# Kernel optimization log

Hardware: AMD Instinct MI355X
Metric: run time of the kernel (lower is better)

The kernel has to match this reference:

```python
import jax, jax.numpy as jnp
import numpy as np

K = 1024       # num mixture components
D = 6          # state_dim (pos + vel)
B = 16384      # number of query points


def setup_inputs() -> dict:
    key = jax.random.key(0)
    k1, k2, k3, k4 = jax.random.split(key, 4)
    x = jax.random.normal(k1, (B, D), dtype=jnp.float32)
    means = jax.random.normal(k2, (K, D), dtype=jnp.float32)
    # SPD covariances: F @ F^T / D + 0.1 * I
    F = jax.random.normal(k3, (K, D, D), dtype=jnp.float32)
    covs = jnp.einsum('kij,klj->kil', F, F) / D + 0.1 * jnp.eye(D, dtype=jnp.float32)
    w = jax.random.uniform(k4, (K,), dtype=jnp.float32, minval=0.1, maxval=1.0)
    weights = w / jnp.sum(w)
    return {"x": x, "means": means, "covs": covs, "weights": weights}


def reference(x, means, covs, weights):
    """Batched GMM.log_pdf: for each point x_b, logsumexp_k [log w_k + log N(x_b; mu_k, Sigma_k)].
    Same math as the equinox module (Cholesky + triangular solve per component),
    vectorized over both components and query points.
    Returns log_pdf of shape [B]."""
    L = jnp.linalg.cholesky(covs)                      # [K, D, D]
    diff = x[:, None, :] - means[None, :, :]           # [B, K, D]
    # Solve L_k y = diff for all points at once: b has shape [K, D, B]
    b = jnp.transpose(diff, (1, 2, 0))                 # [K, D, B]
    y = jax.scipy.linalg.solve_triangular(L, b, lower=True)  # [K, D, B]
    quad = jnp.sum(y * y, axis=1)                      # [K, B]
    log_det = 2.0 * jnp.sum(jnp.log(jnp.diagonal(L, axis1=-2, axis2=-1)), axis=-1)  # [K]
    k_dim = means.shape[-1]
    log_prob = -0.5 * (k_dim * jnp.log(2.0 * jnp.pi) + log_det[:, None] + quad)      # [K, B]
    log_comp = jnp.log(weights)[:, None] + log_prob    # [K, B]
    return jax.scipy.special.logsumexp(log_comp, axis=0)  # [B]
```

## Files before the change

kernel.cpp:

```cpp
#include <hip/hip_runtime.h>
#include <hip/hip_bf16.h>
#include <math.h>

#define KCOMP 1024
#define DDIM  6
#define BPTS  16384

#define SPLIT 16
#define CPT   (KCOMP/SPLIT)
#define PTS   64
#define NCOEF 28

__global__ void gmm_precompute(const float* __restrict__ means,
                               const float* __restrict__ covs,
                               const float* __restrict__ weights,
                               float* __restrict__ coefs) {
    int k = blockIdx.x * blockDim.x + threadIdx.x;
    if (k >= KCOMP) return;

    float A[6][6];
    const float* C = covs + k * 36;
    #pragma unroll
    for (int i = 0; i < 6; i++)
        #pragma unroll
        for (int j = 0; j < 6; j++)
            A[i][j] = C[i * 6 + j];

    float L[6][6];
    #pragma unroll
    for (int j = 0; j < 6; j++) {
        float d = A[j][j];
        #pragma unroll
        for (int t = 0; t < 6; t++) if (t < j) d -= L[j][t] * L[j][t];
        float ljj = sqrtf(d);
        L[j][j] = ljj;
        float inv = 1.0f / ljj;
        #pragma unroll
        for (int i = 0; i < 6; i++) {
            if (i > j) {
                float s = A[i][j];
                #pragma unroll
                for (int t = 0; t < 6; t++) if (t < j) s -= L[i][t] * L[j][t];
                L[i][j] = s * inv;
            }
        }
    }

    float Li[6][6];
    #pragma unroll
    for (int j = 0; j < 6; j++) {
        Li[j][j] = 1.0f / L[j][j];
        #pragma unroll
        for (int i = 0; i < 6; i++) {
            if (i > j) {
                float s = 0.0f;
                #pragma unroll
                for (int t = 0; t < 6; t++) if (t >= j && t < i) s += L[i][t] * Li[t][j];
                Li[i][j] = -s / L[i][i];
            }
        }
    }

    float P[6][6];
    #pragma unroll
    for (int i = 0; i < 6; i++) {
        #pragma unroll
        for (int j = 0; j < 6; j++) {
            if (j >= i) {
                float s = 0.0f;
                int lo = (i > j) ? i : j;
                #pragma unroll
                for (int t = 0; t < 6; t++) if (t >= lo) s += Li[t][i] * Li[t][j];
                P[i][j] = s;
                P[j][i] = s;
            }
        }
    }

    float logdet = 0.0f;
    #pragma unroll
    for (int i = 0; i < 6; i++) logdet += logf(L[i][i]);
    logdet *= 2.0f;

    const float* mu = means + k * 6;
    float m[6];
    #pragma unroll
    for (int i = 0; i < 6; i++) m[i] = mu[i];

    float b[6];
    float muPmu = 0.0f;
    #pragma unroll
    for (int i = 0; i < 6; i++) {
        float s = 0.0f;
        #pragma unroll
        for (int j = 0; j < 6; j++) s += P[i][j] * m[j];
        b[i] = s;
        muPmu += s * m[i];
    }

    const float LOG_2PI = 1.8378770664093453f;
    const float LOG2E   = 1.4426950408889634f;
    float c = logf(weights[k]) - 0.5f * (6.0f * LOG_2PI + logdet) - 0.5f * muPmu;

    float* cf = coefs + k * NCOEF;
    int t = 0;
    #pragma unroll
    for (int i = 0; i < 6; i++)
        #pragma unroll
        for (int j = 0; j < 6; j++)
            if (j >= i) cf[t++] = LOG2E * ((i == j) ? -0.5f * P[i][j] : -P[i][j]);
    #pragma unroll
    for (int i = 0; i < 6; i++) cf[t++] = LOG2E * b[i];
    cf[27] = LOG2E * c;
}

__global__ __launch_bounds__(1024, 4) void gmm_main(const float* __restrict__ x,
                                                    const float* __restrict__ coefs,
                                                    float* __restrict__ out) {
    const int lane = threadIdx.x & 63;
    const int wave = __builtin_amdgcn_readfirstlane((int)(threadIdx.x >> 6));
    const int p = blockIdx.x * PTS + lane;

    float xv[6];
    const float* xp = x + p * 6;
    #pragma unroll
    for (int i = 0; i < 6; i++) xv[i] = xp[i];

    float z[27];
    {
        int t = 0;
        #pragma unroll
        for (int i = 0; i < 6; i++)
            #pragma unroll
            for (int j = 0; j < 6; j++)
                if (j >= i) z[t++] = xv[i] * xv[j];
        #pragma unroll
        for (int i = 0; i < 6; i++) z[t++] = xv[i];
    }

    float s0 = 0.0f, s1 = 0.0f;
    const float* cf = coefs + (size_t)wave * CPT * NCOEF;

    #pragma unroll 2
    for (int j = 0; j < CPT; j++) {
        float v0 = cf[27];
        float v1 = 0.0f;
        float v2 = 0.0f;
        #pragma unroll
        for (int t = 0; t < 9; t++)  v0 = fmaf(cf[t],      z[t],      v0);
        #pragma unroll
        for (int t = 0; t < 9; t++)  v1 = fmaf(cf[t + 9],  z[t + 9],  v1);
        #pragma unroll
        for (int t = 0; t < 9; t++)  v2 = fmaf(cf[t + 18], z[t + 18], v2);
        cf += NCOEF;
        float v = (v0 + v1) + v2;
        float e = __builtin_amdgcn_exp2f(v);
        if (j & 1) s1 += e; else s0 += e;
    }

    __shared__ float ss[SPLIT][PTS];
    ss[wave][lane] = s0 + s1;
    __syncthreads();

    if (threadIdx.x < PTS) {
        float S = 0.0f;
        #pragma unroll
        for (int c = 0; c < SPLIT; c++) S += ss[c][lane];
        const float LN2 = 0.6931471805599453f;
        out[p] = LN2 * __builtin_amdgcn_logf(S);
    }
}

extern "C" void kernel_launch(void* const* d_in, const int* in_sizes, int n_in,
                              void* d_out, int out_size, void* d_ws, size_t ws_size,
                              hipStream_t stream) {
    const float* x       = (const float*)d_in[0];
    const float* means   = (const float*)d_in[1];
    const float* covs    = (const float*)d_in[2];
    const float* weights = (const float*)d_in[3];
    float* out = (float*)d_out;
    float* coefs = (float*)d_ws;

    gmm_precompute<<<KCOMP / 256, 256, 0, stream>>>(means, covs, weights, coefs);
    gmm_main<<<BPTS / PTS, 1024, 0, stream>>>(x, coefs, out);
}
```

Measured before the change: 80.92 us.

## Software-prefetch coefficient rows as float4 and spread precompute across more blocks

```diff
diff --git a/kernel.cpp b/kernel.cpp
--- a/kernel.cpp
+++ b/kernel.cpp
@@ -11,11 +11,12 @@
 #define PTS   64
 #define NCOEF 28
 
-__global__ void gmm_precompute(const float* __restrict__ means,
-                               const float* __restrict__ covs,
-                               const float* __restrict__ weights,
-                               float* __restrict__ coefs) {
-    int k = blockIdx.x * blockDim.x + threadIdx.x;
+__global__ __launch_bounds__(64, 1) void gmm_precompute(
+        const float* __restrict__ means,
+        const float* __restrict__ covs,
+        const float* __restrict__ weights,
+        float* __restrict__ coefs) {
+    int k = blockIdx.x * 64 + threadIdx.x;
     if (k >= KCOMP) return;
 
     float A[6][6];
@@ -26,42 +27,44 @@
         for (int j = 0; j < 6; j++)
             A[i][j] = C[i * 6 + j];
 
-    float L[6][6];
+    float logdet = 0.0f;
     #pragma unroll
     for (int j = 0; j < 6; j++) {
         float d = A[j][j];
         #pragma unroll
-        for (int t = 0; t < 6; t++) if (t < j) d -= L[j][t] * L[j][t];
+        for (int t = 0; t < 6; t++) if (t < j) d -= A[j][t] * A[j][t];
         float ljj = sqrtf(d);
-        L[j][j] = ljj;
+        logdet += logf(ljj);
+        A[j][j] = ljj;
         float inv = 1.0f / ljj;
         #pragma unroll
         for (int i = 0; i < 6; i++) {
             if (i > j) {
                 float s = A[i][j];
                 #pragma unroll
-                for (int t = 0; t < 6; t++) if (t < j) s -= L[i][t] * L[j][t];
-                L[i][j] = s * inv;
+                for (int t = 0; t < 6; t++) if (t < j) s -= A[i][t] * A[j][t];
+                A[i][j] = s * inv;
             }
         }
     }
+    logdet *= 2.0f;
 
     float Li[6][6];
     #pragma unroll
     for (int j = 0; j < 6; j++) {
-        Li[j][j] = 1.0f / L[j][j];
+        float invd = 1.0f / A[j][j];
+        Li[j][j] = invd;
         #pragma unroll
         for (int i = 0; i < 6; i++) {
             if (i > j) {
                 float s = 0.0f;
                 #pragma unroll
-                for (int t = 0; t < 6; t++) if (t >= j && t < i) s += L[i][t] * Li[t][j];
-                Li[i][j] = -s / L[i][i];
+                for (int t = 0; t < 6; t++) if (t >= j && t < i) s += A[i][t] * Li[t][j];
+                Li[i][j] = -s * (1.0f / A[i][i]);
             }
         }
     }
 
-    float P[6][6];
     #pragma unroll
     for (int i = 0; i < 6; i++) {
         #pragma unroll
@@ -71,17 +74,12 @@
                 int lo = (i > j) ? i : j;
                 #pragma unroll
                 for (int t = 0; t < 6; t++) if (t >= lo) s += Li[t][i] * Li[t][j];
-                P[i][j] = s;
-                P[j][i] = s;
+                A[i][j] = s;
+                A[j][i] = s;
             }
         }
     }
 
-    float logdet = 0.0f;
-    #pragma unroll
-    for (int i = 0; i < 6; i++) logdet += logf(L[i][i]);
-    logdet *= 2.0f;
-
     const float* mu = means + k * 6;
     float m[6];
     #pragma unroll
@@ -93,7 +91,7 @@
     for (int i = 0; i < 6; i++) {
         float s = 0.0f;
         #pragma unroll
-        for (int j = 0; j < 6; j++) s += P[i][j] * m[j];
+        for (int j = 0; j < 6; j++) s += A[i][j] * m[j];
         b[i] = s;
         muPmu += s * m[i];
     }
@@ -108,10 +106,38 @@
     for (int i = 0; i < 6; i++)
         #pragma unroll
         for (int j = 0; j < 6; j++)
-            if (j >= i) cf[t++] = LOG2E * ((i == j) ? -0.5f * P[i][j] : -P[i][j]);
+            if (j >= i) cf[t++] = LOG2E * ((i == j) ? -0.5f * A[i][j] : -A[i][j]);
     #pragma unroll
     for (int i = 0; i < 6; i++) cf[t++] = LOG2E * b[i];
     cf[27] = LOG2E * c;
+}
+
+struct C7 { float4 v[7]; };
+
+__device__ __forceinline__ C7 ld7(const float4* __restrict__ p) {
+    C7 c;
+    #pragma unroll
+    for (int i = 0; i < 7; i++) c.v[i] = p[i];
+    return c;
+}
+
+__device__ __forceinline__ float dot27(const C7& c, const float* __restrict__ z) {
+    float cfa[28];
+    #pragma unroll
+    for (int i = 0; i < 7; i++) {
+        cfa[4 * i + 0] = c.v[i].x;
+        cfa[4 * i + 1] = c.v[i].y;
+        cfa[4 * i + 2] = c.v[i].z;
+        cfa[4 * i + 3] = c.v[i].w;
+    }
+    float v0 = cfa[27], v1 = 0.0f, v2 = 0.0f;
+    #pragma unroll
+    for (int t = 0; t < 9; t++)  v0 = fmaf(cfa[t],      z[t],      v0);
+    #pragma unroll
+    for (int t = 0; t < 9; t++)  v1 = fmaf(cfa[t + 9],  z[t + 9],  v1);
+    #pragma unroll
+    for (int t = 0; t < 9; t++)  v2 = fmaf(cfa[t + 18], z[t + 18], v2);
+    return (v0 + v1) + v2;
 }
 
 __global__ __launch_bounds__(1024, 4) void gmm_main(const float* __restrict__ x,
@@ -138,25 +164,19 @@
         for (int i = 0; i < 6; i++) z[t++] = xv[i];
     }
 
+    const float4* cf4 = (const float4*)(coefs + (size_t)wave * CPT * NCOEF);
+
     float s0 = 0.0f, s1 = 0.0f;
-    const float* cf = coefs + (size_t)wave * CPT * NCOEF;
+    C7 cur = ld7(cf4);
 
     #pragma unroll 2
-    for (int j = 0; j < CPT; j++) {
-        float v0 = cf[27];
-        float v1 = 0.0f;
-        float v2 = 0.0f;
-        #pragma unroll
-        for (int t = 0; t < 9; t++)  v0 = fmaf(cf[t],      z[t],      v0);
-        #pragma unroll
-        for (int t = 0; t < 9; t++)  v1 = fmaf(cf[t + 9],  z[t + 9],  v1);
-        #pragma unroll
-        for (int t = 0; t < 9; t++)  v2 = fmaf(cf[t + 18], z[t + 18], v2);
-        cf += NCOEF;
-        float v = (v0 + v1) + v2;
-        float e = __builtin_amdgcn_exp2f(v);
+    for (int j = 0; j < CPT - 1; j++) {
+        C7 nxt = ld7(cf4 + (j + 1) * 7);
+        float e = __builtin_amdgcn_exp2f(dot27(cur, z));
         if (j & 1) s1 += e; else s0 += e;
-    }
+        cur = nxt;
+    }
+    s0 += __builtin_amdgcn_exp2f(dot27(cur, z));
 
     __shared__ float ss[SPLIT][PTS];
     ss[wave][lane] = s0 + s1;
@@ -181,6 +201,6 @@
     float* out = (float*)d_out;
     float* coefs = (float*)d_ws;
 
-    gmm_precompute<<<KCOMP / 256, 256, 0, stream>>>(means, covs, weights, coefs);
+    gmm_precompute<<<KCOMP / 64, 64, 0, stream>>>(means, covs, weights, coefs);
     gmm_main<<<BPTS / PTS, 1024, 0, stream>>>(x, coefs, out);
 }
```

Measured after the change: 84.25 us. +4.1%, slower.
